# Performance work log

Hardware: AMD Instinct MI355X
Metric: run time of the kernel (lower is better)

Reference implementation:

```python
import jax, jax.numpy as jnp
import numpy as np

BETA = 0.9
TH = 1.0
SLOPE = 25.0  # fast-sigmoid surrogate slope (spike_grad_slope)

@jax.custom_vjp
def spike_fn(m):
    # Heaviside on (mem - threshold)
    return (m > 0).astype(m.dtype)

def _spike_fwd(m):
    return spike_fn(m), m

def _spike_bwd(m, g):
    # fast-sigmoid surrogate gradient: 1 / (slope*|m| + 1)^2
    return (g / (SLOPE * jnp.abs(m) + 1.0) ** 2,)

spike_fn.defvjp(_spike_fwd, _spike_bwd)


def setup_inputs() -> dict:
    key = jax.random.key(0)
    k1, k2, k3 = jax.random.split(key, 3)
    T, B, I, H, O = 128, 8192, 2, 256, 2
    x = jax.random.normal(k1, (T, B, I), dtype=jnp.float32)
    # xavier_uniform with gain=1: limit = sqrt(6/(fan_in+fan_out))
    lim1 = float(np.sqrt(6.0 / (I + H)))
    lim2 = float(np.sqrt(6.0 / (H + O)))
    W1 = jax.random.uniform(k2, (H, I), jnp.float32, -lim1, lim1)
    W2 = jax.random.uniform(k3, (O, H), jnp.float32, -lim2, lim2)
    return {"x": x, "W1": W1, "W2": W2}


def reference(x, W1, W2):
    # Precompute all per-step input currents in one GEMM: [T,B,H]
    cur = jnp.einsum('tbi,hi->tbh', x, W1)
    B, H = cur.shape[1], cur.shape[2]
    mem0 = jnp.zeros((B, H), cur.dtype)

    def step(mem, c):
        # snntorch Leaky (reset_mechanism='subtract'):
        # reset based on PREVIOUS mem's spike, then leaky integrate, then fire
        reset = spike_fn(mem - TH)
        mem_new = BETA * mem + c - reset * TH
        spk = spike_fn(mem_new - TH)
        # original code detaches mem between steps (1-step truncated BPTT)
        return jax.lax.stop_gradient(mem_new), spk

    _, spk_rec = jax.lax.scan(step, mem0, cur)  # spk_rec: [T,B,H]
    spk_avg = spk_rec[-10:].mean(0)             # [B,H]
    out = jnp.einsum('bh,oh->bo', spk_avg, W2)  # [B,O]
    return out
```

## Files before the change

### kernel.cpp

```cpp
#include <hip/hip_runtime.h>


#define T_STEPS 128
#define BATCH   8192
#define IN_N    2
#define HID     256
#define OUT_N   2
#define TAIL    10

__global__ __launch_bounds__(256) void snn_fwd(const float* __restrict__ x,
                                               const float* __restrict__ W1,
                                               const float* __restrict__ W2,
                                               float* __restrict__ out) {
    const int b = blockIdx.x;
    const int h = threadIdx.x;

    const float w0 = W1[2 * h];
    const float w1 = W1[2 * h + 1];

    const float* xb = x + (size_t)b * IN_N;

    float mem   = 0.0f;
    float spike = 0.0f;
    float cnt   = 0.0f;

#pragma unroll 8
    for (int t = 0; t < T_STEPS - TAIL; ++t) {
        const float x0 = xb[(size_t)t * (BATCH * IN_N)];
        const float x1 = xb[(size_t)t * (BATCH * IN_N) + 1];
        const float c = __fadd_rn(__fmul_rn(x0, w0), __fmul_rn(x1, w1));
        mem   = __fsub_rn(__fadd_rn(__fmul_rn(0.9f, mem), c), spike);
        spike = (mem > 1.0f) ? 1.0f : 0.0f;
    }
#pragma unroll
    for (int t = T_STEPS - TAIL; t < T_STEPS; ++t) {
        const float x0 = xb[(size_t)t * (BATCH * IN_N)];
        const float x1 = xb[(size_t)t * (BATCH * IN_N) + 1];
        const float c = __fadd_rn(__fmul_rn(x0, w0), __fmul_rn(x1, w1));
        mem   = __fsub_rn(__fadd_rn(__fmul_rn(0.9f, mem), c), spike);
        spike = (mem > 1.0f) ? 1.0f : 0.0f;
        cnt += spike;
    }

    const float avg = cnt / 10.0f;

    float p0 = avg * W2[h];
    float p1 = avg * W2[HID + h];

#pragma unroll
    for (int off = 32; off > 0; off >>= 1) {
        p0 += __shfl_down(p0, off, 64);
        p1 += __shfl_down(p1, off, 64);
    }

    __shared__ float s0[4], s1[4];
    const int wave = h >> 6;
    const int lane = h & 63;
    if (lane == 0) { s0[wave] = p0; s1[wave] = p1; }
    __syncthreads();
    if (h == 0) {
        out[(size_t)b * OUT_N + 0] = ((s0[0] + s0[1]) + (s0[2] + s0[3]));
        out[(size_t)b * OUT_N + 1] = ((s1[0] + s1[1]) + (s1[2] + s1[3]));
    }
}

extern "C" void kernel_launch(void* const* d_in, const int* in_sizes, int n_in,
                              void* d_out, int out_size, void* d_ws, size_t ws_size,
                              hipStream_t stream) {
    const float* x  = (const float*)d_in[0];
    const float* W1 = (const float*)d_in[1];
    const float* W2 = (const float*)d_in[2];
    float* out = (float*)d_out;

    snn_fwd<<<BATCH, HID, 0, stream>>>(x, W1, W2, out);
}
```

Measured before the change: 126.8 us.

## Process eight batch rows per block with x staged in shared memory

Each block now handles eight batch elements. It first copies their x time series into shared memory using vectorized loads, then runs eight independent membrane recurrences per thread. This removes the per-step dependent global loads and exposes instruction-level parallelism across the eight chains. The cost is higher register use, a larger shared footprint, and eight times fewer blocks.

```diff
diff --git a/kernel.cpp b/kernel.cpp
--- a/kernel.cpp
+++ b/kernel.cpp
@@ -7,60 +7,100 @@
 #define HID     256
 #define OUT_N   2
 #define TAIL    10
+#define R       8
 
 __global__ __launch_bounds__(256) void snn_fwd(const float* __restrict__ x,
                                                const float* __restrict__ W1,
                                                const float* __restrict__ W2,
                                                float* __restrict__ out) {
-    const int b = blockIdx.x;
-    const int h = threadIdx.x;
+    const int h  = threadIdx.x;
+    const int b0 = blockIdx.x * R;
+
+    __shared__ float sx[T_STEPS * R * IN_N];
+    __shared__ float red[4][R][OUT_N];
+
+    {
+        const float4* xg = (const float4*)x + (size_t)blockIdx.x * (R * IN_N / 4);
+        float4* s4w = (float4*)sx;
+        for (int j = h; j < T_STEPS * 4; j += 256) {
+            const int t = j >> 2, k = j & 3;
+            s4w[j] = xg[(size_t)t * (BATCH * IN_N / 4) + k];
+        }
+    }
+    __syncthreads();
 
     const float w0 = W1[2 * h];
     const float w1 = W1[2 * h + 1];
 
-    const float* xb = x + (size_t)b * IN_N;
+    float mem[R], spk[R], cnt[R];
+#pragma unroll
+    for (int r = 0; r < R; ++r) { mem[r] = 0.0f; spk[r] = 0.0f; cnt[r] = 0.0f; }
 
-    float mem   = 0.0f;
-    float spike = 0.0f;
-    float cnt   = 0.0f;
+    const float4* s4 = (const float4*)sx;
 
-#pragma unroll 8
-    for (int t = 0; t < T_STEPS - TAIL; ++t) {
-        const float x0 = xb[(size_t)t * (BATCH * IN_N)];
-        const float x1 = xb[(size_t)t * (BATCH * IN_N) + 1];
-        const float c = __fadd_rn(__fmul_rn(x0, w0), __fmul_rn(x1, w1));
-        mem   = __fsub_rn(__fadd_rn(__fmul_rn(0.9f, mem), c), spike);
-        spike = (mem > 1.0f) ? 1.0f : 0.0f;
-    }
-#pragma unroll
-    for (int t = T_STEPS - TAIL; t < T_STEPS; ++t) {
-        const float x0 = xb[(size_t)t * (BATCH * IN_N)];
-        const float x1 = xb[(size_t)t * (BATCH * IN_N) + 1];
-        const float c = __fadd_rn(__fmul_rn(x0, w0), __fmul_rn(x1, w1));
-        mem   = __fsub_rn(__fadd_rn(__fmul_rn(0.9f, mem), c), spike);
-        spike = (mem > 1.0f) ? 1.0f : 0.0f;
-        cnt += spike;
+#define STEP(r, xa, xb)                                                          \
+    {                                                                            \
+        const float c = __fadd_rn(__fmul_rn((xa), w0), __fmul_rn((xb), w1));     \
+        mem[r] = __fsub_rn(__fadd_rn(__fmul_rn(0.9f, mem[r]), c), spk[r]);       \
+        spk[r] = (mem[r] > 1.0f) ? 1.0f : 0.0f;                                  \
     }
 
-    const float avg = cnt / 10.0f;
+#pragma unroll 2
+    for (int t = 0; t < T_STEPS - TAIL; ++t) {
+        const float4 q0 = s4[t * 4 + 0];
+        const float4 q1 = s4[t * 4 + 1];
+        const float4 q2 = s4[t * 4 + 2];
+        const float4 q3 = s4[t * 4 + 3];
+        STEP(0, q0.x, q0.y) STEP(1, q0.z, q0.w)
+        STEP(2, q1.x, q1.y) STEP(3, q1.z, q1.w)
+        STEP(4, q2.x, q2.y) STEP(5, q2.z, q2.w)
+        STEP(6, q3.x, q3.y) STEP(7, q3.z, q3.w)
+    }
+#pragma unroll 2
+    for (int t = T_STEPS - TAIL; t < T_STEPS; ++t) {
+        const float4 q0 = s4[t * 4 + 0];
+        const float4 q1 = s4[t * 4 + 1];
+        const float4 q2 = s4[t * 4 + 2];
+        const float4 q3 = s4[t * 4 + 3];
+        STEP(0, q0.x, q0.y) STEP(1, q0.z, q0.w)
+        STEP(2, q1.x, q1.y) STEP(3, q1.z, q1.w)
+        STEP(4, q2.x, q2.y) STEP(5, q2.z, q2.w)
+        STEP(6, q3.x, q3.y) STEP(7, q3.z, q3.w)
+#pragma unroll
+        for (int r = 0; r < R; ++r) cnt[r] += spk[r];
+    }
+#undef STEP
 
-    float p0 = avg * W2[h];
-    float p1 = avg * W2[HID + h];
+    const float w2a = W2[h];
+    const float w2b = W2[HID + h];
+    float p0[R], p1[R];
+#pragma unroll
+    for (int r = 0; r < R; ++r) {
+        const float avg = cnt[r] / 10.0f;
+        p0[r] = avg * w2a;
+        p1[r] = avg * w2b;
+    }
 
 #pragma unroll
     for (int off = 32; off > 0; off >>= 1) {
-        p0 += __shfl_down(p0, off, 64);
-        p1 += __shfl_down(p1, off, 64);
+#pragma unroll
+        for (int r = 0; r < R; ++r) {
+            p0[r] += __shfl_down(p0[r], off, 64);
+            p1[r] += __shfl_down(p1[r], off, 64);
+        }
     }
 
-    __shared__ float s0[4], s1[4];
     const int wave = h >> 6;
     const int lane = h & 63;
-    if (lane == 0) { s0[wave] = p0; s1[wave] = p1; }
+    if (lane == 0) {
+#pragma unroll
+        for (int r = 0; r < R; ++r) { red[wave][r][0] = p0[r]; red[wave][r][1] = p1[r]; }
+    }
     __syncthreads();
-    if (h == 0) {
-        out[(size_t)b * OUT_N + 0] = ((s0[0] + s0[1]) + (s0[2] + s0[3]));
-        out[(size_t)b * OUT_N + 1] = ((s1[0] + s1[1]) + (s1[2] + s1[3]));
+    if (h < R * OUT_N) {
+        const int r = h >> 1, o = h & 1;
+        out[(size_t)(b0 + r) * OUT_N + o] =
+            (red[0][r][o] + red[1][r][o]) + (red[2][r][o] + red[3][r][o]);
     }
 }
 
@@ -72,5 +112,5 @@
     const float* W2 = (const float*)d_in[2];
     float* out = (float*)d_out;
 
-    snn_fwd<<<BATCH, HID, 0, stream>>>(x, W1, W2, out);
+    snn_fwd<<<BATCH / R, HID, 0, stream>>>(x, W1, W2, out);
 }
```

Result: faster. 109.1 us (-14.0%).
